# Kernel tuning notes

Measured on AMD Instinct MI355X. Metric: run time of the kernel, lower is better.

Reference implementation:

```python
import jax, jax.numpy as jnp
import numpy as np

B = 1024          # batch
INPUT_LEN = 4096  # dense width of incoming activation
OUT = 4096        # out_features
FAN_IN = 128      # in_features (fixed fan-in per output)


def setup_inputs() -> dict:
    key = jax.random.key(0)
    k1, k2, k3, k4 = jax.random.split(key, 4)
    bound = 1.0 / np.sqrt(FAN_IN)
    inp = jax.random.normal(k1, (B, INPUT_LEN), dtype=jnp.float32)
    weight = jax.random.uniform(k2, (OUT, FAN_IN), dtype=jnp.float32, minval=-bound, maxval=bound)
    bias = jax.random.uniform(k3, (OUT,), dtype=jnp.float32, minval=-bound, maxval=bound)
    indx_seqs = jax.random.randint(k4, (OUT, FAN_IN), 0, INPUT_LEN, dtype=jnp.int64 if jax.config.jax_enable_x64 else jnp.int32)
    return {"input": inp, "weight": weight, "bias": bias, "indx_seqs": indx_seqs}


def reference(input, weight, bias, indx_seqs):
    # gathered: (B, OUT, FAN_IN); weight broadcast over batch; reduce fan-in.
    gathered = input[:, indx_seqs]
    out = jnp.einsum('of,bof->bo', weight, gathered) + bias
    return out
```

## Files before the change

### kernel.cpp

```cpp
#include <hip/hip_runtime.h>
#include <stdint.h>

#define NB    1024
#define IL    4096
#define NOUT  4096
#define FI    128
#define BTILE 8
#define OSPLIT 4
#define OTILE (NOUT / OSPLIT)
#define SLAB_DW (IL * (BTILE / 2))

__device__ __forceinline__ uint32_t rne_bf16_hi(float x) {
  uint32_t u = __float_as_uint(x);
  u += 0x7FFFu + ((u >> 16) & 1u);
  return u & 0xFFFF0000u;
}

__global__ __launch_bounds__(256)
void pack_kernel(const int* __restrict__ idx, const float* __restrict__ w,
                 uint32_t* __restrict__ pack) {
  int i = blockIdx.x * 256 + threadIdx.x;
  pack[i] = rne_bf16_hi(w[i]) | (((uint32_t)idx[i] << 4) & 0xFFFFu);
}

__global__ __launch_bounds__(256)
void slab_kernel(const float* __restrict__ in, uint32_t* __restrict__ slab) {
  int t = blockIdx.x * 256 + threadIdx.x;
  int g = t >> 12;
  int i = t & (IL - 1);
  const float* base = in + (size_t)g * (8 * IL) + i;
  uint4 v;
  v.x = rne_bf16_hi(base[1 * IL]) | (rne_bf16_hi(base[0 * IL]) >> 16);
  v.y = rne_bf16_hi(base[3 * IL]) | (rne_bf16_hi(base[2 * IL]) >> 16);
  v.z = rne_bf16_hi(base[5 * IL]) | (rne_bf16_hi(base[4 * IL]) >> 16);
  v.w = rne_bf16_hi(base[7 * IL]) | (rne_bf16_hi(base[6 * IL]) >> 16);
  reinterpret_cast<uint4*>(slab)[t] = v;
}

template<int MODE>
__global__ __launch_bounds__(1024)
void lincond_kernel(const float* __restrict__ input,
                    const uint32_t* __restrict__ slab,
                    const uint32_t* __restrict__ pack,
                    const int*  __restrict__ idxs,
                    const float* __restrict__ wgt,
                    const float* __restrict__ bias,
                    float* __restrict__ out) {
  __shared__ uint32_t lds[SLAB_DW];
  const int bid   = blockIdx.x;
  const int b0    = (bid >> 2) * BTILE;
  const int obase = (bid & 3) * OTILE;
  const int tid   = threadIdx.x;

  if (MODE == 2) {
    const uint32_t* src = slab + (size_t)(b0 >> 3) * SLAB_DW;
    #pragma unroll
    for (int r = 0; r < 4; ++r) {
      int e = (r * 1024 + tid) * 4;
      __builtin_amdgcn_global_load_lds(
          (const __attribute__((address_space(1))) uint32_t*)(src + e),
          (__attribute__((address_space(3))) uint32_t*)(lds + e),
          16, 0, 0);
    }
  } else {
    #pragma unroll
    for (int rep = 0; rep < 16; ++rep) {
      int e = rep * 1024 + tid;
      int d = e >> 12;
      int i = e & (IL - 1);
      float x0 = input[(size_t)(b0 + 2 * d)     * IL + i];
      float x1 = input[(size_t)(b0 + 2 * d + 1) * IL + i];
      lds[i * 4 + d] = rne_bf16_hi(x1) | (rne_bf16_hi(x0) >> 16);
    }
  }
  __syncthreads();

  const int o = obase + tid;
  const char* ldsb = reinterpret_cast<const char*>(lds);
  float acc[8] = {0.f,0.f,0.f,0.f,0.f,0.f,0.f,0.f};

#define GBODY(OFF, WV) {                                          \
    uint4 g = *reinterpret_cast<const uint4*>(ldsb + (OFF));      \
    float wv = (WV);                                              \
    acc[0] = fmaf(wv, __uint_as_float(g.x << 16),         acc[0]);\
    acc[1] = fmaf(wv, __uint_as_float(g.x & 0xFFFF0000u), acc[1]);\
    acc[2] = fmaf(wv, __uint_as_float(g.y << 16),         acc[2]);\
    acc[3] = fmaf(wv, __uint_as_float(g.y & 0xFFFF0000u), acc[3]);\
    acc[4] = fmaf(wv, __uint_as_float(g.z << 16),         acc[4]);\
    acc[5] = fmaf(wv, __uint_as_float(g.z & 0xFFFF0000u), acc[5]);\
    acc[6] = fmaf(wv, __uint_as_float(g.w << 16),         acc[6]);\
    acc[7] = fmaf(wv, __uint_as_float(g.w & 0xFFFF0000u), acc[7]);}

#define PBODY(P) \
    GBODY((P.x & 0xFFFFu), __uint_as_float(P.x & 0xFFFF0000u)) \
    GBODY((P.y & 0xFFFFu), __uint_as_float(P.y & 0xFFFF0000u)) \
    GBODY((P.z & 0xFFFFu), __uint_as_float(P.z & 0xFFFF0000u)) \
    GBODY((P.w & 0xFFFFu), __uint_as_float(P.w & 0xFFFF0000u))

#define RBODY(IV, WV) \
    GBODY(((uint32_t)IV.x << 4), WV.x) \
    GBODY(((uint32_t)IV.y << 4), WV.y) \
    GBODY(((uint32_t)IV.z << 4), WV.z) \
    GBODY(((uint32_t)IV.w << 4), WV.w)

  if (MODE >= 1) {
    const uint4* pw = reinterpret_cast<const uint4*>(pack) + (size_t)o * (FI / 4);
    #pragma unroll 2
    for (int j = 0; j < 8; ++j) {
      uint4 p0 = pw[j * 4 + 0];
      uint4 p1 = pw[j * 4 + 1];
      uint4 p2 = pw[j * 4 + 2];
      uint4 p3 = pw[j * 4 + 3];
      PBODY(p0) PBODY(p1) PBODY(p2) PBODY(p3)
    }
  } else {
    const int4*   ip = reinterpret_cast<const int4*>(idxs)  + (size_t)o * (FI / 4);
    const float4* wp = reinterpret_cast<const float4*>(wgt) + (size_t)o * (FI / 4);
    #pragma unroll 2
    for (int j = 0; j < 8; ++j) {
      int4   i0 = ip[j * 4 + 0], i1 = ip[j * 4 + 1], i2 = ip[j * 4 + 2], i3 = ip[j * 4 + 3];
      float4 w0 = wp[j * 4 + 0], w1 = wp[j * 4 + 1], w2 = wp[j * 4 + 2], w3 = wp[j * 4 + 3];
      RBODY(i0, w0) RBODY(i1, w1) RBODY(i2, w2) RBODY(i3, w3)
    }
  }

  const float bv = bias[o];
  #pragma unroll
  for (int k = 0; k < 8; ++k) {
    out[(size_t)(b0 + k) * NOUT + o] = acc[k] + bv;
  }
}

extern "C" void kernel_launch(void* const* d_in, const int* in_sizes, int n_in,
                              void* d_out, int out_size, void* d_ws, size_t ws_size,
                              hipStream_t stream) {
  const float* input  = (const float*)d_in[0];
  const float* weight = (const float*)d_in[1];
  const float* bias   = (const float*)d_in[2];
  const int*   idxs   = (const int*)d_in[3];
  float*       out    = (float*)d_out;

  const size_t pack_bytes = (size_t)NOUT * FI * sizeof(uint32_t);
  const size_t slab_bytes = (size_t)(NB / BTILE) * SLAB_DW * sizeof(uint32_t);
  const int grid = (NB / BTILE) * OSPLIT;

  if (ws_size >= pack_bytes + slab_bytes) {
    uint32_t* pack = (uint32_t*)d_ws;
    uint32_t* slab = (uint32_t*)((char*)d_ws + pack_bytes);
    pack_kernel<<<(NOUT * FI) / 256, 256, 0, stream>>>(idxs, weight, pack);
    slab_kernel<<<(NB / BTILE) * IL / 256, 256, 0, stream>>>(input, slab);
    lincond_kernel<2><<<grid, 1024, 0, stream>>>(input, slab, pack, nullptr, nullptr, bias, out);
  } else if (ws_size >= pack_bytes) {
    uint32_t* pack = (uint32_t*)d_ws;
    pack_kernel<<<(NOUT * FI) / 256, 256, 0, stream>>>(idxs, weight, pack);
    lincond_kernel<1><<<grid, 1024, 0, stream>>>(input, nullptr, pack, nullptr, nullptr, bias, out);
  } else {
    lincond_kernel<0><<<grid, 1024, 0, stream>>>(input, nullptr, nullptr, idxs, weight, bias, out);
  }
}
```

Baseline: 57.37 us.

## Fuse prep kernels and reorder fan-in entries by LDS bank group with rotation

Merges the pack and slab preparation kernels into a single launch, saving one kernel launch. Within each output row, the packed weight/index entries are counting-sorted by a 3-bit bank field taken from the LDS offset, then rotated per output. This spreads simultaneous 16-byte LDS gathers across lanes over different banks to cut bank conflicts. The inner loop also drops the masking of low bits on the bf16 halves, which accepts small extra error from the leftover index and neighbour bits in the mantissa. The MODE 1 fallback path is removed.

```diff
diff --git a/kernel.cpp b/kernel.cpp
--- a/kernel.cpp
+++ b/kernel.cpp
@@ -9,6 +9,8 @@
 #define OSPLIT 4
 #define OTILE (NOUT / OSPLIT)
 #define SLAB_DW (IL * (BTILE / 2))
+#define SLAB_BLOCKS ((NB / BTILE) * IL / 256)
+#define SORT_BLOCKS (NOUT / 4)
 
 __device__ __forceinline__ uint32_t rne_bf16_hi(float x) {
   uint32_t u = __float_as_uint(x);
@@ -17,24 +19,46 @@
 }
 
 __global__ __launch_bounds__(256)
-void pack_kernel(const int* __restrict__ idx, const float* __restrict__ w,
+void prep_kernel(const float* __restrict__ in, uint32_t* __restrict__ slab,
+                 const int* __restrict__ idx, const float* __restrict__ w,
                  uint32_t* __restrict__ pack) {
-  int i = blockIdx.x * 256 + threadIdx.x;
-  pack[i] = rne_bf16_hi(w[i]) | (((uint32_t)idx[i] << 4) & 0xFFFFu);
-}
-
-__global__ __launch_bounds__(256)
-void slab_kernel(const float* __restrict__ in, uint32_t* __restrict__ slab) {
-  int t = blockIdx.x * 256 + threadIdx.x;
-  int g = t >> 12;
-  int i = t & (IL - 1);
-  const float* base = in + (size_t)g * (8 * IL) + i;
-  uint4 v;
-  v.x = rne_bf16_hi(base[1 * IL]) | (rne_bf16_hi(base[0 * IL]) >> 16);
-  v.y = rne_bf16_hi(base[3 * IL]) | (rne_bf16_hi(base[2 * IL]) >> 16);
-  v.z = rne_bf16_hi(base[5 * IL]) | (rne_bf16_hi(base[4 * IL]) >> 16);
-  v.w = rne_bf16_hi(base[7 * IL]) | (rne_bf16_hi(base[6 * IL]) >> 16);
-  reinterpret_cast<uint4*>(slab)[t] = v;
+  const int bid = blockIdx.x;
+  if (bid < SLAB_BLOCKS) {
+    int t = bid * 256 + threadIdx.x;
+    int g = t >> 12;
+    int i = t & (IL - 1);
+    const float* base = in + (size_t)g * (8 * IL) + i;
+    uint4 v;
+    v.x = rne_bf16_hi(base[1 * IL]) | (rne_bf16_hi(base[0 * IL]) >> 16);
+    v.y = rne_bf16_hi(base[3 * IL]) | (rne_bf16_hi(base[2 * IL]) >> 16);
+    v.z = rne_bf16_hi(base[5 * IL]) | (rne_bf16_hi(base[4 * IL]) >> 16);
+    v.w = rne_bf16_hi(base[7 * IL]) | (rne_bf16_hi(base[6 * IL]) >> 16);
+    reinterpret_cast<uint4*>(slab)[t] = v;
+  } else {
+    const int o    = (bid - SLAB_BLOCKS) * 4 + (threadIdx.x >> 6);
+    const unsigned lane = threadIdx.x & 63u;
+    const float* wrow = w   + (size_t)o * FI;
+    const int*   irow = idx + (size_t)o * FI;
+    uint32_t p0 = rne_bf16_hi(wrow[lane])      | (((uint32_t)irow[lane]      << 4) & 0xFFFFu);
+    uint32_t p1 = rne_bf16_hi(wrow[64 + lane]) | (((uint32_t)irow[64 + lane] << 4) & 0xFFFFu);
+    uint32_t k0 = (p0 >> 4) & 7u, k1 = (p1 >> 4) & 7u;
+    uint64_t lt = (lane == 63u) ? 0x7FFFFFFFFFFFFFFFull : ((1ull << (lane + 1)) - 1) >> 1;
+    uint32_t run = 0, base0 = 0, base1 = 0, c0k1 = 0;
+    uint64_t match0 = 0, match1 = 0;
+    #pragma unroll
+    for (int k = 0; k < 8; ++k) {
+      uint64_t b0 = __ballot(k0 == (uint32_t)k);
+      uint64_t b1 = __ballot(k1 == (uint32_t)k);
+      if (k0 == (uint32_t)k) { base0 = run; match0 = b0; }
+      if (k1 == (uint32_t)k) { base1 = run; match1 = b1; c0k1 = (uint32_t)__popcll(b0); }
+      run += (uint32_t)__popcll(b0) + (uint32_t)__popcll(b1);
+    }
+    uint32_t pos0 = base0 + (uint32_t)__popcll(match0 & lt);
+    uint32_t pos1 = base1 + c0k1 + (uint32_t)__popcll(match1 & lt);
+    uint32_t rot  = 2u * (uint32_t)(o & 63);
+    pack[(size_t)o * FI + ((pos0 + rot) & 127u)] = p0;
+    pack[(size_t)o * FI + ((pos1 + rot) & 127u)] = p1;
+  }
 }
 
 template<int MODE>
@@ -82,20 +106,20 @@
 #define GBODY(OFF, WV) {                                          \
     uint4 g = *reinterpret_cast<const uint4*>(ldsb + (OFF));      \
     float wv = (WV);                                              \
-    acc[0] = fmaf(wv, __uint_as_float(g.x << 16),         acc[0]);\
-    acc[1] = fmaf(wv, __uint_as_float(g.x & 0xFFFF0000u), acc[1]);\
-    acc[2] = fmaf(wv, __uint_as_float(g.y << 16),         acc[2]);\
-    acc[3] = fmaf(wv, __uint_as_float(g.y & 0xFFFF0000u), acc[3]);\
-    acc[4] = fmaf(wv, __uint_as_float(g.z << 16),         acc[4]);\
-    acc[5] = fmaf(wv, __uint_as_float(g.z & 0xFFFF0000u), acc[5]);\
-    acc[6] = fmaf(wv, __uint_as_float(g.w << 16),         acc[6]);\
-    acc[7] = fmaf(wv, __uint_as_float(g.w & 0xFFFF0000u), acc[7]);}
+    acc[0] = fmaf(wv, __uint_as_float(g.x << 16), acc[0]);        \
+    acc[1] = fmaf(wv, __uint_as_float(g.x),       acc[1]);        \
+    acc[2] = fmaf(wv, __uint_as_float(g.y << 16), acc[2]);        \
+    acc[3] = fmaf(wv, __uint_as_float(g.y),       acc[3]);        \
+    acc[4] = fmaf(wv, __uint_as_float(g.z << 16), acc[4]);        \
+    acc[5] = fmaf(wv, __uint_as_float(g.z),       acc[5]);        \
+    acc[6] = fmaf(wv, __uint_as_float(g.w << 16), acc[6]);        \
+    acc[7] = fmaf(wv, __uint_as_float(g.w),       acc[7]);}
 
 #define PBODY(P) \
-    GBODY((P.x & 0xFFFFu), __uint_as_float(P.x & 0xFFFF0000u)) \
-    GBODY((P.y & 0xFFFFu), __uint_as_float(P.y & 0xFFFF0000u)) \
-    GBODY((P.z & 0xFFFFu), __uint_as_float(P.z & 0xFFFF0000u)) \
-    GBODY((P.w & 0xFFFFu), __uint_as_float(P.w & 0xFFFF0000u))
+    GBODY((P.x & 0xFFFFu), __uint_as_float(P.x)) \
+    GBODY((P.y & 0xFFFFu), __uint_as_float(P.y)) \
+    GBODY((P.z & 0xFFFFu), __uint_as_float(P.z)) \
+    GBODY((P.w & 0xFFFFu), __uint_as_float(P.w))
 
 #define RBODY(IV, WV) \
     GBODY(((uint32_t)IV.x << 4), WV.x) \
@@ -147,13 +171,8 @@
   if (ws_size >= pack_bytes + slab_bytes) {
     uint32_t* pack = (uint32_t*)d_ws;
     uint32_t* slab = (uint32_t*)((char*)d_ws + pack_bytes);
-    pack_kernel<<<(NOUT * FI) / 256, 256, 0, stream>>>(idxs, weight, pack);
-    slab_kernel<<<(NB / BTILE) * IL / 256, 256, 0, stream>>>(input, slab);
+    prep_kernel<<<SLAB_BLOCKS + SORT_BLOCKS, 256, 0, stream>>>(input, slab, idxs, weight, pack);
     lincond_kernel<2><<<grid, 1024, 0, stream>>>(input, slab, pack, nullptr, nullptr, bias, out);
-  } else if (ws_size >= pack_bytes) {
-    uint32_t* pack = (uint32_t*)d_ws;
-    pack_kernel<<<(NOUT * FI) / 256, 256, 0, stream>>>(idxs, weight, pack);
-    lincond_kernel<1><<<grid, 1024, 0, stream>>>(input, nullptr, pack, nullptr, nullptr, bias, out);
   } else {
     lincond_kernel<0><<<grid, 1024, 0, stream>>>(input, nullptr, nullptr, idxs, weight, bias, out);
   }
```

Result: slower. 73.55 us (+28.2%).
